# Kernel tuning notes

Measured on AMD Instinct MI355X. Metric: run time of the kernel, lower is better.

## Reference

```python
import jax, jax.numpy as jnp
import numpy as np

B, S, HID = 2, 2048, 2048
NH, NKV, D = 16, 4, 128
EPS = 1e-6
THETA = 1000000.0
SCALE = D ** -0.5


def _rmsnorm(x, w):
    # per-head RMSNorm over last dim (head_dim)
    var = jnp.mean(x * x, axis=-1, keepdims=True)
    return x * jax.lax.rsqrt(var + EPS) * w


def _rope(pos, x):
    # neox-style rotary over full head_dim. x: [B,S,h,D], pos: [B,S]
    half = D // 2
    inv_freq = THETA ** (-jnp.arange(half, dtype=jnp.float32) / half)  # theta^(-2i/D)
    freqs = pos.astype(jnp.float32)[..., None] * inv_freq              # [B,S,half]
    cos = jnp.cos(freqs)[:, :, None, :]
    sin = jnp.sin(freqs)[:, :, None, :]
    x1, x2 = x[..., :half], x[..., half:]
    return jnp.concatenate([x1 * cos - x2 * sin, x2 * cos + x1 * sin], axis=-1)


def setup_inputs() -> dict:
    key = jax.random.key(0)
    ks = jax.random.split(key, 6)
    hidden_states = jax.random.normal(ks[0], (B, S, HID), dtype=jnp.float32)
    positions = jnp.tile(jnp.arange(S, dtype=jnp.int32)[None, :], (B, 1))
    sd = 0.02
    Wq = jax.random.normal(ks[1], (HID, NH * D), dtype=jnp.float32) * sd
    Wk = jax.random.normal(ks[2], (HID, NKV * D), dtype=jnp.float32) * sd
    Wv = jax.random.normal(ks[3], (HID, NKV * D), dtype=jnp.float32) * sd
    Wo = jax.random.normal(ks[4], (NH * D, HID), dtype=jnp.float32) * sd
    q_norm_w = jnp.ones((D,), dtype=jnp.float32)
    k_norm_w = jnp.ones((D,), dtype=jnp.float32)
    return {"hidden_states": hidden_states, "positions": positions,
            "Wq": Wq, "Wk": Wk, "Wv": Wv, "Wo": Wo,
            "q_norm_w": q_norm_w, "k_norm_w": k_norm_w}


def reference(hidden_states, positions, Wq, Wk, Wv, Wo, q_norm_w, k_norm_w):
    # QKV projections (no bias)
    q = (hidden_states @ Wq).reshape(B, S, NH, D)
    k = (hidden_states @ Wk).reshape(B, S, NKV, D)
    v = (hidden_states @ Wv).reshape(B, S, NKV, D)
    # per-head RMSNorm
    q = _rmsnorm(q, q_norm_w)
    k = _rmsnorm(k, k_norm_w)
    # rotary embedding
    q = _rope(positions, q)
    k = _rope(positions, k)
    # GQA: expand kv heads to q heads
    rep = NH // NKV
    k = jnp.repeat(k, rep, axis=2)  # [B,S,NH,D]
    v = jnp.repeat(v, rep, axis=2)
    # non-causal (ENCODER_ONLY) attention
    scores = jnp.einsum('bqhd,bkhd->bhqk', q, k) * SCALE
    attn = jax.nn.softmax(scores, axis=-1)
    ctx = jnp.einsum('bhqk,bkhd->bqhd', attn, v).reshape(B, S, NH * D)
    out = ctx @ Wo
    return out
```

## Files before the change

kernel.cpp:

```cpp
#include <hip/hip_runtime.h>

typedef unsigned short ushort_t;
typedef __attribute__((ext_vector_type(8))) short short8;
typedef __attribute__((ext_vector_type(4))) float f32x4;

#define Bb 2
#define Ss 2048
#define HID 2048
#define NH 16
#define NKV 4
#define Dd 128
constexpr float EPS_ = 1e-6f;
constexpr float THETA_ = 1000000.0f;
constexpr float SCALE_ = 0.08838834764831845f;
constexpr float C2_ = 0.12753785f;
constexpr float THR_RAW_ = 23.5f;

__device__ __forceinline__ ushort_t f2bf(float x) {
  union { float f; unsigned u; } v; v.f = x;
  unsigned r = (v.u + 0x7fffu + ((v.u >> 16) & 1u)) >> 16;
  return (ushort_t)r;
}
__device__ __forceinline__ float bf2f(ushort_t u) {
  union { unsigned u; float f; } v; v.u = ((unsigned)u) << 16;
  return v.f;
}

typedef const __attribute__((address_space(1))) void* gas1_t;
typedef __attribute__((address_space(3))) void* las3_t;
__device__ __forceinline__ void gload_lds16(const void* g, void* l) {
  __builtin_amdgcn_global_load_lds((gas1_t)g, (las3_t)l, 16, 0, 0);
}

__device__ __forceinline__ void store_out(float* p, float v) { *p = v; }
__device__ __forceinline__ void store_out(ushort_t* p, float v) { *p = f2bf(v); }

__global__ __launch_bounds__(256) void convert_f32_bf16(
    const float* __restrict__ src, ushort_t* __restrict__ dst, long n) {
  long i = ((long)blockIdx.x * 256 + threadIdx.x) * 4;
  if (i + 3 < n) {
    float4 v = *(const float4*)(src + i);
    ushort_t o0 = f2bf(v.x), o1 = f2bf(v.y), o2 = f2bf(v.z), o3 = f2bf(v.w);
    ushort_t* d = dst + i;
    d[0] = o0; d[1] = o1; d[2] = o2; d[3] = o3;
  }
}

__global__ __launch_bounds__(256) void transpose_f32_bf16(
    const float* __restrict__ src, ushort_t* __restrict__ dst, int R, int C) {
  __shared__ float tile[32][33];
  int c0 = blockIdx.x * 32, r0 = blockIdx.y * 32;
  int tx = threadIdx.x & 31, ty = threadIdx.x >> 5;
#pragma unroll
  for (int j = 0; j < 4; j++)
    tile[ty + j * 8][tx] = src[(long)(r0 + ty + j * 8) * C + c0 + tx];
  __syncthreads();
#pragma unroll
  for (int j = 0; j < 4; j++)
    dst[(long)(c0 + ty + j * 8) * R + r0 + tx] = f2bf(tile[tx][ty + j * 8]);
}

template <typename OutT>
__global__ __launch_bounds__(256) void gemm_bt(
    const ushort_t* __restrict__ A, const ushort_t* __restrict__ Bt,
    OutT* __restrict__ C, int M, int N, int K) {
  __shared__ __align__(16) ushort_t As[128 * 32];
  __shared__ __align__(16) ushort_t Bs[128 * 32];
  const int t = threadIdx.x;
  const int wave = t >> 6, lane = t & 63;
  const int wr = wave >> 1, wc = wave & 1;
  const int quad = lane >> 4, l16 = lane & 15;

  unsigned gx = gridDim.x;
  unsigned nwg = gx * gridDim.y;
  unsigned lin = blockIdx.y * gx + blockIdx.x;
  if ((nwg & 7u) == 0u) {
    unsigned cpx = nwg >> 3;
    lin = (lin & 7u) * cpx + (lin >> 3);
  }
  const long bm = (long)(lin / gx) * 128;
  const long bn = (long)(lin % gx) * 128;

  f32x4 acc[4][4] = {};

  const int srow = t >> 2, schunk = t & 3;
  const ushort_t* aSrc = A + (bm + srow) * (long)K + schunk * 8;
  const ushort_t* bSrc = Bt + (bn + srow) * (long)K + schunk * 8;
  const int ldsOff = srow * 32 + schunk * 8;

  for (int k0 = 0; k0 < K; k0 += 32) {
    __syncthreads();
    gload_lds16(aSrc + k0, &As[ldsOff]);
    gload_lds16(aSrc + (long)64 * K + k0, &As[ldsOff + 64 * 32]);
    gload_lds16(bSrc + k0, &Bs[ldsOff]);
    gload_lds16(bSrc + (long)64 * K + k0, &Bs[ldsOff + 64 * 32]);
    __syncthreads();
    short8 af[4], bf[4];
#pragma unroll
    for (int i = 0; i < 4; i++) {
      af[i] = *(const short8*)&As[(wr * 64 + i * 16 + l16) * 32 + quad * 8];
      bf[i] = *(const short8*)&Bs[(wc * 64 + i * 16 + l16) * 32 + quad * 8];
    }
#pragma unroll
    for (int i = 0; i < 4; i++)
#pragma unroll
      for (int j = 0; j < 4; j++)
        acc[i][j] = __builtin_amdgcn_mfma_f32_16x16x32_bf16(af[i], bf[j], acc[i][j], 0, 0, 0);
  }
#pragma unroll
  for (int i = 0; i < 4; i++)
#pragma unroll
    for (int j = 0; j < 4; j++)
#pragma unroll
      for (int r = 0; r < 4; r++) {
        long rr = bm + wr * 64 + i * 16 + quad * 4 + r;
        long cc = bn + wc * 64 + j * 16 + l16;
        store_out(&C[rr * N + cc], acc[i][j][r]);
      }
}

__global__ __launch_bounds__(256) void rmsnorm_rope(
    ushort_t* __restrict__ qkv, const int* __restrict__ positions,
    const float* __restrict__ qw, const float* __restrict__ kw) {
  int gw = blockIdx.x * 4 + (threadIdx.x >> 6);
  int lane = threadIdx.x & 63;
  int bs = gw / 20, h = gw % 20;
  ushort_t* src = qkv + (long)bs * 3072 + h * 128;
  float x0 = bf2f(src[lane]), x1 = bf2f(src[lane + 64]);
  float ss = x0 * x0 + x1 * x1;
#pragma unroll
  for (int off = 32; off; off >>= 1) ss += __shfl_xor(ss, off);
  float r = rsqrtf(ss * (1.0f / 128.0f) + EPS_);
  const float* w = (h < 16) ? qw : kw;
  x0 = x0 * r * w[lane];
  x1 = x1 * r * w[lane + 64];
  float pos = (float)positions[bs];
  float inv_freq = powf(THETA_, -(float)lane * (1.0f / 64.0f));
  float f = pos * inv_freq;
  float sn, cs;
  sincosf(f, &sn, &cs);
  float o0 = x0 * cs - x1 * sn;
  float o1 = x1 * cs + x0 * sn;
  src[lane] = f2bf(o0);
  src[lane + 64] = f2bf(o1);
}

__global__ __launch_bounds__(256) void transpose_v(
    const ushort_t* __restrict__ qkv, ushort_t* __restrict__ Vt) {
  __shared__ ushort_t tile[64][65];
  int bh = blockIdx.z;
  int s0 = blockIdx.x * 64, d0 = blockIdx.y * 64;
  int b = bh >> 2, hk = bh & 3;
  int tx = threadIdx.x & 63, ty = threadIdx.x >> 6;
#pragma unroll
  for (int j = 0; j < 16; j++) {
    int sl = j * 4 + ty;
    tile[sl][tx] = qkv[(long)(b * Ss + s0 + sl) * 3072 + 2560 + hk * 128 + d0 + tx];
  }
  __syncthreads();
  const long vtbase = (long)bh * Dd * Ss;
#pragma unroll
  for (int j = 0; j < 16; j++) {
    int dl = j * 4 + ty;
    Vt[vtbase + (long)(d0 + dl) * Ss + s0 + tx] = tile[tx][dl];
  }
}

__global__ __launch_bounds__(512) void flash_attn(
    const ushort_t* __restrict__ qkv, const ushort_t* __restrict__ Vt,
    ushort_t* __restrict__ ctx) {
  __shared__ __align__(16) ushort_t Ks[2][64 * 128];
  __shared__ __align__(16) ushort_t Vs[2][128 * 64];
  __shared__ __align__(16) ushort_t Ps[8][16 * 64];
  const int qt = blockIdx.x, h = blockIdx.y, b = blockIdx.z;
  const int hk = h >> 2;
  const int t = threadIdx.x, wave = t >> 6, lane = t & 63;
  const int quad = lane >> 4, l16 = lane & 15;

  const ushort_t* qp = qkv + (long)(b * Ss + qt * 128) * 3072 + h * 128;
  const ushort_t* kp = qkv + (long)(b * Ss) * 3072 + 2048 + hk * 128;
  const ushort_t* vp = Vt + ((long)(b * NKV + hk) * Dd) * Ss;

  auto stage = [&](int kt, int bi) {
    const int k0 = kt * 64;
#pragma unroll
    for (int it = 0; it < 2; it++) {
      int tt = t + it * 512;
      int row = tt >> 4, cl = tt & 15, cg = cl ^ (row & 15);
      gload_lds16(kp + (long)(k0 + row) * 3072 + cg * 8, &Ks[bi][tt * 8]);
    }
#pragma unroll
    for (int it = 0; it < 2; it++) {
      int tt = t + it * 512;
      int row = tt >> 3, cl = tt & 7, cg = cl ^ (row & 7);
      gload_lds16(vp + (long)row * Ss + k0 + cg * 8, &Vs[bi][tt * 8]);
    }
  };

  stage(0, 0);

  short8 qf[4];
  {
    const ushort_t* qrow = qp + (long)(wave * 16 + l16) * 3072 + quad * 8;
#pragma unroll
    for (int kc = 0; kc < 4; kc++)
      qf[kc] = *(const short8*)(qrow + kc * 32);
  }

  float m_i = -1e30f;
  float l_acc = 0.f;
  f32x4 o[8] = {};

  asm volatile("s_waitcnt vmcnt(0)" ::: "memory");
  __syncthreads();

  int cur = 0;
  for (int kt = 0; kt < Ss / 64; kt++) {
    if (kt + 1 < Ss / 64) stage(kt + 1, cur ^ 1);

    f32x4 sa[4] = {};
    __builtin_amdgcn_s_setprio(1);
#pragma unroll
    for (int kc = 0; kc < 4; kc++) {
#pragma unroll
      for (int nt = 0; nt < 4; nt++) {
        int brow = nt * 16 + l16;
        short8 kfr = *(const short8*)&Ks[cur][brow * 128 + (((kc * 4 + quad) ^ (brow & 15)) * 8)];
        sa[nt] = __builtin_amdgcn_mfma_f32_16x16x32_bf16(kfr, qf[kc], sa[nt], 0, 0, 0);
      }
    }
    __builtin_amdgcn_s_setprio(0);

    float pmax = sa[0][0];
#pragma unroll
    for (int nt = 0; nt < 4; nt++)
#pragma unroll
      for (int r = 0; r < 4; r++) pmax = fmaxf(pmax, sa[nt][r]);

    bool upd = __any(pmax > m_i + THR_RAW_);
    float alpha = 1.0f;
    if (upd) {
      float mx = fmaxf(pmax, __shfl_xor(pmax, 16));
      mx = fmaxf(mx, __shfl_xor(mx, 32));
      float mnew = fmaxf(m_i, mx);
      alpha = __builtin_amdgcn_exp2f((m_i - mnew) * C2_);
      m_i = mnew;
      l_acc *= alpha;
    }

    float mC2 = m_i * C2_;
    float rs = 0.f;
#pragma unroll
    for (int nt = 0; nt < 4; nt++) {
      int cbase = l16 * 64 + ((nt * 2 + (quad >> 1)) ^ (l16 & 7)) * 8 + (quad & 1) * 4;
#pragma unroll
      for (int r = 0; r < 4; r++) {
        float p = __builtin_amdgcn_exp2f(__builtin_fmaf(sa[nt][r], C2_, -mC2));
        rs += p;
        union { float f; unsigned u; } pv; pv.f = p;
        Ps[wave][cbase + r] = (ushort_t)((pv.u + 0x8000u) >> 16);
      }
    }
    l_acc += rs;

    if (upd) {
      float ar0 = __shfl(alpha, quad * 4 + 0);
      float ar1 = __shfl(alpha, quad * 4 + 1);
      float ar2 = __shfl(alpha, quad * 4 + 2);
      float ar3 = __shfl(alpha, quad * 4 + 3);
#pragma unroll
      for (int dt = 0; dt < 8; dt++) {
        o[dt][0] *= ar0; o[dt][1] *= ar1; o[dt][2] *= ar2; o[dt][3] *= ar3;
      }
    }
    asm volatile("s_waitcnt lgkmcnt(0)" ::: "memory");

    __builtin_amdgcn_s_setprio(1);
#pragma unroll
    for (int kc = 0; kc < 2; kc++) {
      int arow = l16;
      short8 af = *(const short8*)&Ps[wave][arow * 64 + (((kc * 4 + quad) ^ (arow & 7)) * 8)];
#pragma unroll
      for (int dt = 0; dt < 8; dt++) {
        int brow = dt * 16 + l16;
        short8 bfr = *(const short8*)&Vs[cur][brow * 64 + (((kc * 4 + quad) ^ (brow & 7)) * 8)];
        o[dt] = __builtin_amdgcn_mfma_f32_16x16x32_bf16(af, bfr, o[dt], 0, 0, 0);
      }
    }
    __builtin_amdgcn_s_setprio(0);

    asm volatile("s_waitcnt vmcnt(0)" ::: "memory");
    __syncthreads();
    cur ^= 1;
  }

  float lt = l_acc + __shfl_xor(l_acc, 16);
  lt += __shfl_xor(lt, 32);
  float linv = 1.0f / lt;
  float lr0 = __shfl(linv, quad * 4 + 0);
  float lr1 = __shfl(linv, quad * 4 + 1);
  float lr2 = __shfl(linv, quad * 4 + 2);
  float lr3 = __shfl(linv, quad * 4 + 3);
  const long obase = (long)(b * Ss + qt * 128 + wave * 16) * (NH * Dd) + h * Dd;
#pragma unroll
  for (int dt = 0; dt < 8; dt++) {
    int col = dt * 16 + l16;
    ctx[obase + (long)(quad * 4 + 0) * (NH * Dd) + col] = f2bf(o[dt][0] * lr0);
    ctx[obase + (long)(quad * 4 + 1) * (NH * Dd) + col] = f2bf(o[dt][1] * lr1);
    ctx[obase + (long)(quad * 4 + 2) * (NH * Dd) + col] = f2bf(o[dt][2] * lr2);
    ctx[obase + (long)(quad * 4 + 3) * (NH * Dd) + col] = f2bf(o[dt][3] * lr3);
  }
}

extern "C" void kernel_launch(void* const* d_in, const int* in_sizes, int n_in,
                              void* d_out, int out_size, void* d_ws, size_t ws_size,
                              hipStream_t stream) {
  const float* hidden = (const float*)d_in[0];
  const int* positions = (const int*)d_in[1];
  const float* Wq = (const float*)d_in[2];
  const float* Wk = (const float*)d_in[3];
  const float* Wv = (const float*)d_in[4];
  const float* Wo = (const float*)d_in[5];
  const float* qw = (const float*)d_in[6];
  const float* kw = (const float*)d_in[7];
  float* out = (float*)d_out;

  char* ws = (char*)d_ws;
  ushort_t* Xbf = (ushort_t*)(ws);
  ushort_t* WqkvT = (ushort_t*)(ws + (16l << 20));
  ushort_t* WoT = (ushort_t*)(ws + (28l << 20));
  ushort_t* qkvb = (ushort_t*)(ws + (36l << 20));
  ushort_t* Vt = (ushort_t*)(ws + (60l << 20));
  ushort_t* ctx = Xbf;

  const long nX = (long)Bb * Ss * HID;
  convert_f32_bf16<<<(unsigned)(nX / 4 / 256), 256, 0, stream>>>(hidden, Xbf, nX);
  transpose_f32_bf16<<<dim3(2048 / 32, 2048 / 32), 256, 0, stream>>>(Wq, WqkvT, 2048, 2048);
  transpose_f32_bf16<<<dim3(512 / 32, 2048 / 32), 256, 0, stream>>>(Wk, WqkvT + (long)2048 * 2048, 2048, 512);
  transpose_f32_bf16<<<dim3(512 / 32, 2048 / 32), 256, 0, stream>>>(Wv, WqkvT + (long)2560 * 2048, 2048, 512);
  transpose_f32_bf16<<<dim3(2048 / 32, 2048 / 32), 256, 0, stream>>>(Wo, WoT, 2048, 2048);

  gemm_bt<ushort_t><<<dim3(3072 / 128, 4096 / 128), 256, 0, stream>>>(Xbf, WqkvT, qkvb, 4096, 3072, 2048);

  rmsnorm_rope<<<(Bb * Ss * 20) / 4, 256, 0, stream>>>(qkvb, positions, qw, kw);
  transpose_v<<<dim3(Ss / 64, Dd / 64, Bb * NKV), 256, 0, stream>>>(qkvb, Vt);

  flash_attn<<<dim3(Ss / 128, NH, Bb), 512, 0, stream>>>(qkvb, Vt, ctx);

  gemm_bt<float><<<dim3(2048 / 128, 4096 / 128), 256, 0, stream>>>(ctx, WoT, out, 4096, 2048, 2048);
}
```

Measured before the change: 360.8 us.

## Use 256x256-tile pipelined GEMM with swizzled LDS for QKV projection

Adds a new 512-thread GEMM kernel with 256x256 output tiles, K-step 64, double-buffered LDS filled by direct global-to-LDS loads, XOR-swizzled LDS layout, staged half-tile prefetch interleaved with MFMA phases, s_setprio, and a grouped workgroup remap. The QKV projection now uses it instead of the 128x128 kernel. The goal is more data reuse per block and better overlap of memory loads with MFMA work. The trade-off is only 192 workgroups, fewer than two per CU, plus heavy register and 128KB LDS pressure that limits occupancy.

```diff
diff --git a/kernel.cpp b/kernel.cpp
--- a/kernel.cpp
+++ b/kernel.cpp
@@ -115,6 +115,180 @@
       for (int r = 0; r < 4; r++) {
         long rr = bm + wr * 64 + i * 16 + quad * 4 + r;
         long cc = bn + wc * 64 + j * 16 + l16;
+        store_out(&C[rr * N + cc], acc[i][j][r]);
+      }
+}
+
+template <typename OutT>
+__global__ __launch_bounds__(512) void gemm256_bt(
+    const ushort_t* __restrict__ A, const ushort_t* __restrict__ Bt,
+    OutT* __restrict__ C, int M, int N, int K) {
+  __shared__ __align__(16) ushort_t As[2][256 * 64];
+  __shared__ __align__(16) ushort_t Bs[2][256 * 64];
+  const int t = threadIdx.x;
+  const int wave = t >> 6, lane = t & 63;
+  const int wm = wave >> 2, wn = wave & 3;
+  const int quad = lane >> 4, l16 = lane & 15;
+
+  unsigned gx = gridDim.x;
+  unsigned nwg = gx * gridDim.y;
+  unsigned lin = blockIdx.y * gx + blockIdx.x;
+  if ((nwg & 7u) == 0u) {
+    unsigned cpx = nwg >> 3;
+    lin = (lin & 7u) * cpx + (lin >> 3);
+  }
+  const long bm = (long)(lin / gx) * 256;
+  const long bn = (long)(lin % gx) * 256;
+
+  auto stageA = [&](int kt, int ih, int bi) {
+    const int k0 = kt * 64;
+#pragma unroll
+    for (int it = 0; it < 2; it++) {
+      int ci = t + it * 512;
+      int lr = ci >> 3, cl = ci & 7;
+      int row = ((lr & 64) << 1) | (ih << 6) | (lr & 63);
+      int cg = cl ^ (row & 7);
+      gload_lds16(A + (bm + row) * (long)K + k0 + cg * 8, &As[bi][row * 64 + cl * 8]);
+    }
+  };
+  auto stageB = [&](int kt, int jh, int bi) {
+    const int k0 = kt * 64;
+#pragma unroll
+    for (int it = 0; it < 2; it++) {
+      int ci = t + it * 512;
+      int lr = ci >> 3, cl = ci & 7;
+      int row = ((lr & 96) << 1) | (jh << 5) | (lr & 31);
+      int cg = cl ^ (row & 7);
+      gload_lds16(Bt + (bn + row) * (long)K + k0 + cg * 8, &Bs[bi][row * 64 + cl * 8]);
+    }
+  };
+
+  f32x4 acc[8][4] = {};
+  short8 af[2][4], bf0[2][2], bf1[2][2];
+
+  const int nt = K >> 6;
+  stageA(0, 0, 0); stageA(0, 1, 0); stageB(0, 0, 0); stageB(0, 1, 0);
+  stageA(1, 0, 1); stageB(1, 0, 1);
+  asm volatile("s_waitcnt vmcnt(4)" ::: "memory");
+  __builtin_amdgcn_sched_barrier(0);
+  __builtin_amdgcn_s_barrier();
+  __builtin_amdgcn_sched_barrier(0);
+
+  const int raBase = (wm * 128 + l16) * 64;
+  const int rbBase = (wn * 64 + l16) * 64;
+  const int sw = l16 & 7;
+
+  for (int ti = 0; ti < nt; ti++) {
+    const int cb = ti & 1;
+    const ushort_t* as_ = As[cb];
+    const ushort_t* bs_ = Bs[cb];
+
+#pragma unroll
+    for (int kk = 0; kk < 2; kk++) {
+      int ch = ((kk * 4 + quad) ^ sw) * 8;
+#pragma unroll
+      for (int di = 0; di < 4; di++)
+        af[kk][di] = *(const short8*)&as_[raBase + di * 1024 + ch];
+#pragma unroll
+      for (int dj = 0; dj < 2; dj++)
+        bf0[kk][dj] = *(const short8*)&bs_[rbBase + dj * 1024 + ch];
+    }
+    if (ti + 1 < nt) stageA(ti + 1, 1, cb ^ 1);
+    __builtin_amdgcn_sched_barrier(0);
+    __builtin_amdgcn_s_barrier();
+    __builtin_amdgcn_sched_barrier(0);
+    __builtin_amdgcn_s_setprio(1);
+#pragma unroll
+    for (int di = 0; di < 4; di++)
+#pragma unroll
+      for (int dj = 0; dj < 2; dj++)
+#pragma unroll
+        for (int kk = 0; kk < 2; kk++)
+          acc[di][dj] = __builtin_amdgcn_mfma_f32_16x16x32_bf16(af[kk][di], bf0[kk][dj], acc[di][dj], 0, 0, 0);
+    __builtin_amdgcn_s_setprio(0);
+    __builtin_amdgcn_sched_barrier(0);
+    __builtin_amdgcn_s_barrier();
+    __builtin_amdgcn_sched_barrier(0);
+
+#pragma unroll
+    for (int kk = 0; kk < 2; kk++) {
+      int ch = ((kk * 4 + quad) ^ sw) * 8;
+#pragma unroll
+      for (int dj = 0; dj < 2; dj++)
+        bf1[kk][dj] = *(const short8*)&bs_[rbBase + (2 + dj) * 1024 + ch];
+    }
+    if (ti + 1 < nt) stageB(ti + 1, 1, cb ^ 1);
+    __builtin_amdgcn_sched_barrier(0);
+    __builtin_amdgcn_s_barrier();
+    __builtin_amdgcn_sched_barrier(0);
+    __builtin_amdgcn_s_setprio(1);
+#pragma unroll
+    for (int di = 0; di < 4; di++)
+#pragma unroll
+      for (int dj = 0; dj < 2; dj++)
+#pragma unroll
+        for (int kk = 0; kk < 2; kk++)
+          acc[di][2 + dj] = __builtin_amdgcn_mfma_f32_16x16x32_bf16(af[kk][di], bf1[kk][dj], acc[di][2 + dj], 0, 0, 0);
+    __builtin_amdgcn_s_setprio(0);
+    __builtin_amdgcn_sched_barrier(0);
+    __builtin_amdgcn_s_barrier();
+    __builtin_amdgcn_sched_barrier(0);
+
+#pragma unroll
+    for (int kk = 0; kk < 2; kk++) {
+      int ch = ((kk * 4 + quad) ^ sw) * 8;
+#pragma unroll
+      for (int di = 0; di < 4; di++)
+        af[kk][di] = *(const short8*)&as_[raBase + (4 + di) * 1024 + ch];
+    }
+    if (ti + 2 < nt) stageA(ti + 2, 0, cb);
+    __builtin_amdgcn_sched_barrier(0);
+    __builtin_amdgcn_s_barrier();
+    __builtin_amdgcn_sched_barrier(0);
+    __builtin_amdgcn_s_setprio(1);
+#pragma unroll
+    for (int di = 0; di < 4; di++)
+#pragma unroll
+      for (int dj = 0; dj < 2; dj++)
+#pragma unroll
+        for (int kk = 0; kk < 2; kk++)
+          acc[4 + di][dj] = __builtin_amdgcn_mfma_f32_16x16x32_bf16(af[kk][di], bf0[kk][dj], acc[4 + di][dj], 0, 0, 0);
+    __builtin_amdgcn_s_setprio(0);
+    __builtin_amdgcn_sched_barrier(0);
+    __builtin_amdgcn_s_barrier();
+    __builtin_amdgcn_sched_barrier(0);
+
+    if (ti + 2 < nt) stageB(ti + 2, 0, cb);
+    __builtin_amdgcn_sched_barrier(0);
+    __builtin_amdgcn_s_barrier();
+    __builtin_amdgcn_sched_barrier(0);
+    __builtin_amdgcn_s_setprio(1);
+#pragma unroll
+    for (int di = 0; di < 4; di++)
+#pragma unroll
+      for (int dj = 0; dj < 2; dj++)
+#pragma unroll
+        for (int kk = 0; kk < 2; kk++)
+          acc[4 + di][2 + dj] = __builtin_amdgcn_mfma_f32_16x16x32_bf16(af[kk][di], bf1[kk][dj], acc[4 + di][2 + dj], 0, 0, 0);
+    __builtin_amdgcn_s_setprio(0);
+    if (ti + 2 < nt) {
+      asm volatile("s_waitcnt vmcnt(4)" ::: "memory");
+    } else if (ti + 1 < nt) {
+      asm volatile("s_waitcnt vmcnt(0)" ::: "memory");
+    }
+    __builtin_amdgcn_sched_barrier(0);
+    __builtin_amdgcn_s_barrier();
+    __builtin_amdgcn_sched_barrier(0);
+  }
+
+#pragma unroll
+  for (int i = 0; i < 8; i++)
+#pragma unroll
+    for (int j = 0; j < 4; j++)
+#pragma unroll
+      for (int r = 0; r < 4; r++) {
+        long rr = bm + wm * 128 + i * 16 + quad * 4 + r;
+        long cc = bn + wn * 64 + j * 16 + l16;
         store_out(&C[rr * N + cc], acc[i][j][r]);
       }
 }
@@ -340,7 +514,7 @@
   transpose_f32_bf16<<<dim3(512 / 32, 2048 / 32), 256, 0, stream>>>(Wv, WqkvT + (long)2560 * 2048, 2048, 512);
   transpose_f32_bf16<<<dim3(2048 / 32, 2048 / 32), 256, 0, stream>>>(Wo, WoT, 2048, 2048);
 
-  gemm_bt<ushort_t><<<dim3(3072 / 128, 4096 / 128), 256, 0, stream>>>(Xbf, WqkvT, qkvb, 4096, 3072, 2048);
+  gemm256_bt<ushort_t><<<dim3(3072 / 256, 4096 / 256), 512, 0, stream>>>(Xbf, WqkvT, qkvb, 4096, 3072, 2048);
 
   rmsnorm_rope<<<(Bb * Ss * 20) / 4, 256, 0, stream>>>(qkvb, positions, qw, kw);
   transpose_v<<<dim3(Ss / 64, Dd / 64, Bb * NKV), 256, 0, stream>>>(qkvb, Vt);
```

Result: faster. 349.9 us (-3.0%).
